# Kernel optimization log

Hardware: AMD Instinct MI355X
Metric: run time of the kernel (lower is better)

## Reference

```python
import jax, jax.numpy as jnp
import numpy as np

N, D, E, EDGE_DIM = 50000, 128, 800000, 3
NEG_SLOPE = 0.2
LN_EPS = 1e-5


def setup_inputs() -> dict:
    key = jax.random.key(0)
    ks = jax.random.split(key, 12)
    s = 1.0 / np.sqrt(D)
    return {
        "x": jax.random.normal(ks[0], (N, D), jnp.float32),
        "edge_index": jax.random.randint(ks[1], (2, E), 0, N, jnp.int32),
        "edge_attr": jax.random.normal(ks[2], (E, EDGE_DIM), jnp.float32),
        "W_l": jax.random.normal(ks[3], (D, D), jnp.float32) * s,
        "b_l": jnp.zeros((D,), jnp.float32),
        "W_r": jax.random.normal(ks[4], (D, D), jnp.float32) * s,
        "b_r": jnp.zeros((D,), jnp.float32),
        "W_e": jax.random.normal(ks[5], (EDGE_DIM, D), jnp.float32) * (1.0 / np.sqrt(EDGE_DIM)),
        "att": jax.random.normal(ks[6], (D,), jnp.float32) * s,
        "bias": jnp.zeros((D,), jnp.float32),
        "res_weight": jnp.array(0.1, jnp.float32),
        "ln_gamma": jnp.ones((D,), jnp.float32),
        "ln_beta": jnp.zeros((D,), jnp.float32),
    }


def reference(x, edge_index, edge_attr, W_l, b_l, W_r, b_r, W_e, att, bias,
              res_weight, ln_gamma, ln_beta):
    src, dst = edge_index[0], edge_index[1]
    # GATv2: lin_l on source, lin_r on target (heads=1, concat=False)
    x_l = x @ W_l + b_l            # [N, D]
    x_r = x @ W_r + b_r            # [N, D]
    e_emb = edge_attr @ W_e        # [E, D]
    # per-edge attention logits
    m = x_l[src] + x_r[dst] + e_emb                      # [E, D]
    m = jnp.where(m > 0, m, NEG_SLOPE * m)               # leaky_relu(0.2)
    alpha = m @ att                                       # [E]
    # segment softmax over destination nodes
    seg_max = jax.ops.segment_max(alpha, dst, num_segments=N)
    seg_max = jnp.where(jnp.isfinite(seg_max), seg_max, 0.0)
    ex = jnp.exp(alpha - seg_max[dst])
    seg_sum = jax.ops.segment_sum(ex, dst, num_segments=N)
    alpha = ex / (seg_sum[dst] + 1e-16)                   # [E]
    # weighted aggregation of transformed source features (dropout off / eval)
    msgs = x_l[src] * alpha[:, None]                      # [E, D]
    out = jax.ops.segment_sum(msgs, dst, num_segments=N) + bias  # [N, D]
    # residual + LayerNorm
    out = x + res_weight * out
    mu = jnp.mean(out, axis=-1, keepdims=True)
    var = jnp.mean(jnp.square(out - mu), axis=-1, keepdims=True)
    out = (out - mu) * jax.lax.rsqrt(var + LN_EPS)
    return out * ln_gamma + ln_beta
```

## Files before the change

### kernel.cpp

```cpp
#include <hip/hip_runtime.h>
#include <hip/hip_bf16.h>

#define N_NODES 50000
#define DIM 128
#define N_EDGES 800000
#define NEG_SLOPE 0.2f
#define LN_EPS 1e-5f
#define SCAN_BS 256
#define NB_SCAN ((N_NODES + SCAN_BS - 1) / SCAN_BS)


__global__ __launch_bounds__(256) void lin_kernel(
    const float* __restrict__ x,
    const float* __restrict__ Wl, const float* __restrict__ bl,
    const float* __restrict__ Wr, const float* __restrict__ br,
    __hip_bfloat16* __restrict__ xl_bf, float* __restrict__ xr)
{
    __shared__ float xs[8][DIM];
    const int node0 = blockIdx.x * 8;
    const int t = threadIdx.x;
    for (int i = t; i < 8 * DIM; i += 256) {
        int n = node0 + (i >> 7);
        xs[i >> 7][i & 127] = (n < N_NODES) ? x[(size_t)n * DIM + (i & 127)] : 0.f;
    }
    __syncthreads();
    const int d = t & 127;
    const bool is_l = (t < 128);
    const float* W = is_l ? Wl : Wr;
    const float* b = is_l ? bl : br;
    float acc[8];
#pragma unroll
    for (int i = 0; i < 8; i++) acc[i] = b[d];
    for (int k = 0; k < DIM; k++) {
        float w = W[k * DIM + d];
#pragma unroll
        for (int i = 0; i < 8; i++) acc[i] += xs[i][k] * w;
    }
#pragma unroll
    for (int i = 0; i < 8; i++) {
        int n = node0 + i;
        if (n < N_NODES) {
            if (is_l) xl_bf[(size_t)n * DIM + d] = __float2bfloat16(acc[i]);
            else      xr[(size_t)n * DIM + d] = acc[i];
        }
    }
}

__global__ __launch_bounds__(256) void hist_kernel(const int* __restrict__ dst_idx,
                                                   int* __restrict__ cnt) {
    int e = blockIdx.x * 256 + threadIdx.x;
    if (e < N_EDGES) atomicAdd(&cnt[dst_idx[e]], 1);
}

__global__ __launch_bounds__(SCAN_BS) void scan1_kernel(int* __restrict__ cnt,
                                                        int* __restrict__ partials) {
    __shared__ int sh[SCAN_BS];
    const int i = blockIdx.x * SCAN_BS + threadIdx.x;
    const int v = (i < N_NODES) ? cnt[i] : 0;
    sh[threadIdx.x] = v;
    __syncthreads();
    for (int off = 1; off < SCAN_BS; off <<= 1) {
        int t = (threadIdx.x >= off) ? sh[threadIdx.x - off] : 0;
        __syncthreads();
        sh[threadIdx.x] += t;
        __syncthreads();
    }
    if (i < N_NODES) cnt[i] = sh[threadIdx.x] - v;
    if (threadIdx.x == SCAN_BS - 1) partials[blockIdx.x] = sh[threadIdx.x];
}

__global__ __launch_bounds__(SCAN_BS) void scan2_kernel(int* __restrict__ partials) {
    __shared__ int sh[SCAN_BS];
    const int t = threadIdx.x;
    const int v = (t < NB_SCAN) ? partials[t] : 0;
    sh[t] = v;
    __syncthreads();
    for (int off = 1; off < SCAN_BS; off <<= 1) {
        int u = (t >= off) ? sh[t - off] : 0;
        __syncthreads();
        sh[t] += u;
        __syncthreads();
    }
    if (t < NB_SCAN) partials[t] = sh[t] - v;
}

__global__ __launch_bounds__(SCAN_BS) void scan3_kernel(int* __restrict__ cnt,
                                                        const int* __restrict__ partials) {
    const int i = blockIdx.x * SCAN_BS + threadIdx.x;
    if (i < N_NODES) cnt[i] += partials[blockIdx.x];
}

__global__ __launch_bounds__(256) void scatter_kernel(
    const int* __restrict__ src_idx, const int* __restrict__ dst_idx,
    const float* __restrict__ ea,
    int* __restrict__ cursor,
    int* __restrict__ sorted_src, float* __restrict__ sorted_ea) {
    int e = blockIdx.x * 256 + threadIdx.x;
    if (e >= N_EDGES) return;
    int pos = atomicAdd(&cursor[dst_idx[e]], 1);
    sorted_src[pos] = src_idx[e];
    sorted_ea[3 * pos + 0] = ea[(size_t)e * 3 + 0];
    sorted_ea[3 * pos + 1] = ea[(size_t)e * 3 + 1];
    sorted_ea[3 * pos + 2] = ea[(size_t)e * 3 + 2];
}

__global__ __launch_bounds__(256) void fused_node_kernel(
    const float* __restrict__ x, const __hip_bfloat16* __restrict__ xl_bf,
    const int* __restrict__ cursor,
    const int* __restrict__ sorted_src, const float* __restrict__ sorted_ea,
    const float* __restrict__ We, const float* __restrict__ att,
    const float* __restrict__ bias, const float* __restrict__ rw_p,
    const float* __restrict__ gamma, const float* __restrict__ beta,
    float* __restrict__ out)
{
    const int v = blockIdx.x * 4 + (threadIdx.x >> 6);
    const int lane = threadIdx.x & 63;
    if (v >= N_NODES) return;
    const int begin = (v == 0) ? 0 : cursor[v - 1];
    const int end = cursor[v];
    const size_t nb = (size_t)v * DIM + 2 * lane;
    const float2 xrv = *(const float2*)&out[nb];
    const float2 at  = *(const float2*)&att[2 * lane];
    const float2 we0 = *(const float2*)&We[0 * DIM + 2 * lane];
    const float2 we1 = *(const float2*)&We[1 * DIM + 2 * lane];
    const float2 we2 = *(const float2*)&We[2 * DIM + 2 * lane];

    float m = -3.4e38f, s = 0.f, a0 = 0.f, a1 = 0.f;
    for (int pos = begin; pos < end; ++pos) {
        const int sn = sorted_src[pos];
        const float ea0 = sorted_ea[3 * pos + 0];
        const float ea1 = sorted_ea[3 * pos + 1];
        const float ea2 = sorted_ea[3 * pos + 2];
        const unsigned xu = *(const unsigned*)&xl_bf[(size_t)sn * DIM + 2 * lane];
        const float xl0 = __uint_as_float(xu << 16);
        const float xl1 = __uint_as_float(xu & 0xffff0000u);
        float t0 = xl0 + xrv.x + ea0 * we0.x + ea1 * we1.x + ea2 * we2.x;
        float t1 = xl1 + xrv.y + ea0 * we0.y + ea1 * we1.y + ea2 * we2.y;
        t0 = t0 > 0.f ? t0 : NEG_SLOPE * t0;
        t1 = t1 > 0.f ? t1 : NEG_SLOPE * t1;
        float p = t0 * at.x + t1 * at.y;
#pragma unroll
        for (int o = 32; o > 0; o >>= 1) p += __shfl_xor(p, o, 64);
        const float mn = fmaxf(m, p);
        const float f = expf(m - mn);
        const float w = expf(p - mn);
        s  = s  * f + w;
        a0 = a0 * f + w * xl0;
        a1 = a1 * f + w * xl1;
        m = mn;
    }
    const float inv = 1.f / (s + 1e-16f);

    const float2 xv = *(const float2*)&x[nb];
    const float rw = rw_p[0];
    float v0 = xv.x + rw * (a0 * inv + bias[2 * lane]);
    float v1 = xv.y + rw * (a1 * inv + bias[2 * lane + 1]);
    float sum = v0 + v1;
#pragma unroll
    for (int o = 32; o > 0; o >>= 1) sum += __shfl_xor(sum, o, 64);
    const float mu = sum * (1.f / DIM);
    const float d0 = v0 - mu, d1 = v1 - mu;
    float q = d0 * d0 + d1 * d1;
#pragma unroll
    for (int o = 32; o > 0; o >>= 1) q += __shfl_xor(q, o, 64);
    const float rstd = rsqrtf(q * (1.f / DIM) + LN_EPS);
    float2 r;
    r.x = d0 * rstd * gamma[2 * lane]     + beta[2 * lane];
    r.y = d1 * rstd * gamma[2 * lane + 1] + beta[2 * lane + 1];
    *(float2*)&out[nb] = r;
}

extern "C" void kernel_launch(void* const* d_in, const int* in_sizes, int n_in,
                              void* d_out, int out_size, void* d_ws, size_t ws_size,
                              hipStream_t stream)
{
    const float* x    = (const float*)d_in[0];
    const int*   ei   = (const int*)d_in[1];
    const float* ea   = (const float*)d_in[2];
    const float* Wl   = (const float*)d_in[3];
    const float* bl   = (const float*)d_in[4];
    const float* Wr   = (const float*)d_in[5];
    const float* br   = (const float*)d_in[6];
    const float* We   = (const float*)d_in[7];
    const float* att  = (const float*)d_in[8];
    const float* bias = (const float*)d_in[9];
    const float* rw   = (const float*)d_in[10];
    const float* gmm  = (const float*)d_in[11];
    const float* bta  = (const float*)d_in[12];
    float* out = (float*)d_out;

    const int* src_idx = ei;
    const int* dst_idx = ei + N_EDGES;

    __hip_bfloat16* xl_bf = (__hip_bfloat16*)d_ws;
    int*   sorted_src = (int*)(xl_bf + (size_t)N_NODES * DIM);
    float* sorted_ea  = (float*)(sorted_src + N_EDGES);
    int*   cursor     = (int*)(sorted_ea + (size_t)3 * N_EDGES);
    int*   partials   = cursor + N_NODES + 64;

    hipMemsetAsync(cursor, 0, (size_t)(N_NODES + 64) * sizeof(int), stream);
    hist_kernel<<<(N_EDGES + 255) / 256, 256, 0, stream>>>(dst_idx, cursor);
    scan1_kernel<<<NB_SCAN, SCAN_BS, 0, stream>>>(cursor, partials);
    scan2_kernel<<<1, SCAN_BS, 0, stream>>>(partials);
    scan3_kernel<<<NB_SCAN, SCAN_BS, 0, stream>>>(cursor, partials);
    scatter_kernel<<<(N_EDGES + 255) / 256, 256, 0, stream>>>(src_idx, dst_idx, ea,
                                                              cursor, sorted_src, sorted_ea);
    lin_kernel<<<(N_NODES + 7) / 8, 256, 0, stream>>>(x, Wl, bl, Wr, br, xl_bf, out);
    fused_node_kernel<<<(N_NODES + 3) / 4, 256, 0, stream>>>(x, xl_bf, cursor,
                                                             sorted_src, sorted_ea,
                                                             We, att, bias, rw, gmm, bta, out);
}
```

Measured before the change: 389.9 us.

## Pad CSR rows to multiples of four and batch four edges per iteration

Each node's edge segment is padded to a multiple of four, so the node kernel can read sources and edge attributes with vector loads and process four edges per step. The four per-edge dot-product reductions share one combined shuffle tree instead of four full butterflies. The online softmax skips the rescale when the new logits are within a threshold of the running max, and uses fast __expf. This adds a padded workspace layout and a separate row-start array, and the threshold trick risks exp overflow or precision loss for large logit gaps.

```diff
diff --git a/kernel.cpp b/kernel.cpp
--- a/kernel.cpp
+++ b/kernel.cpp
@@ -8,6 +8,7 @@
 #define LN_EPS 1e-5f
 #define SCAN_BS 256
 #define NB_SCAN ((N_NODES + SCAN_BS - 1) / SCAN_BS)
+#define PADCAP (N_EDGES + 4 * N_NODES)
 
 
 __global__ __launch_bounds__(256) void lin_kernel(
@@ -56,13 +57,14 @@
                                                         int* __restrict__ partials) {
     __shared__ int sh[SCAN_BS];
     const int i = blockIdx.x * SCAN_BS + threadIdx.x;
-    const int v = (i < N_NODES) ? cnt[i] : 0;
+    const int deg = (i < N_NODES) ? cnt[i] : 0;
+    const int v = (deg + 3) & ~3;
     sh[threadIdx.x] = v;
     __syncthreads();
     for (int off = 1; off < SCAN_BS; off <<= 1) {
-        int t = (threadIdx.x >= off) ? sh[threadIdx.x - off] : 0;
-        __syncthreads();
-        sh[threadIdx.x] += t;
+        int u = (threadIdx.x >= off) ? sh[threadIdx.x - off] : 0;
+        __syncthreads();
+        sh[threadIdx.x] += u;
         __syncthreads();
     }
     if (i < N_NODES) cnt[i] = sh[threadIdx.x] - v;
@@ -85,9 +87,14 @@
 }
 
 __global__ __launch_bounds__(SCAN_BS) void scan3_kernel(int* __restrict__ cnt,
-                                                        const int* __restrict__ partials) {
+                                                        const int* __restrict__ partials,
+                                                        int* __restrict__ cursor) {
     const int i = blockIdx.x * SCAN_BS + threadIdx.x;
-    if (i < N_NODES) cnt[i] += partials[blockIdx.x];
+    if (i < N_NODES) {
+        int rs = cnt[i] + partials[blockIdx.x];
+        cnt[i] = rs;
+        cursor[i] = rs;
+    }
 }
 
 __global__ __launch_bounds__(256) void scatter_kernel(
@@ -106,7 +113,7 @@
 
 __global__ __launch_bounds__(256) void fused_node_kernel(
     const float* __restrict__ x, const __hip_bfloat16* __restrict__ xl_bf,
-    const int* __restrict__ cursor,
+    const int* __restrict__ row_start, const int* __restrict__ cursor,
     const int* __restrict__ sorted_src, const float* __restrict__ sorted_ea,
     const float* __restrict__ We, const float* __restrict__ att,
     const float* __restrict__ bias, const float* __restrict__ rw_p,
@@ -116,8 +123,8 @@
     const int v = blockIdx.x * 4 + (threadIdx.x >> 6);
     const int lane = threadIdx.x & 63;
     if (v >= N_NODES) return;
-    const int begin = (v == 0) ? 0 : cursor[v - 1];
-    const int end = cursor[v];
+    const int begin = row_start[v];
+    const int end   = cursor[v];
     const size_t nb = (size_t)v * DIM + 2 * lane;
     const float2 xrv = *(const float2*)&out[nb];
     const float2 at  = *(const float2*)&att[2 * lane];
@@ -126,7 +133,81 @@
     const float2 we2 = *(const float2*)&We[2 * DIM + 2 * lane];
 
     float m = -3.4e38f, s = 0.f, a0 = 0.f, a1 = 0.f;
-    for (int pos = begin; pos < end; ++pos) {
+    int pos = begin;
+
+    for (; pos + 4 <= end; pos += 4) {
+        const int4 s4 = *(const int4*)(sorted_src + pos);
+        const float4* eap = (const float4*)(sorted_ea + 3 * pos);
+        const float4 eA = eap[0], eB = eap[1], eC = eap[2];
+        const unsigned xu0 = *(const unsigned*)&xl_bf[(size_t)s4.x * DIM + 2 * lane];
+        const unsigned xu1 = *(const unsigned*)&xl_bf[(size_t)s4.y * DIM + 2 * lane];
+        const unsigned xu2 = *(const unsigned*)&xl_bf[(size_t)s4.z * DIM + 2 * lane];
+        const unsigned xu3 = *(const unsigned*)&xl_bf[(size_t)s4.w * DIM + 2 * lane];
+        const float xl00 = __uint_as_float(xu0 << 16), xl10 = __uint_as_float(xu0 & 0xffff0000u);
+        const float xl01 = __uint_as_float(xu1 << 16), xl11 = __uint_as_float(xu1 & 0xffff0000u);
+        const float xl02 = __uint_as_float(xu2 << 16), xl12 = __uint_as_float(xu2 & 0xffff0000u);
+        const float xl03 = __uint_as_float(xu3 << 16), xl13 = __uint_as_float(xu3 & 0xffff0000u);
+
+        float P0, P1, P2, P3;
+        {
+            float t0, t1;
+            t0 = xl00 + xrv.x + eA.x * we0.x + eA.y * we1.x + eA.z * we2.x;
+            t1 = xl10 + xrv.y + eA.x * we0.y + eA.y * we1.y + eA.z * we2.y;
+            t0 = t0 > 0.f ? t0 : NEG_SLOPE * t0;  t1 = t1 > 0.f ? t1 : NEG_SLOPE * t1;
+            P0 = t0 * at.x + t1 * at.y;
+            t0 = xl01 + xrv.x + eA.w * we0.x + eB.x * we1.x + eB.y * we2.x;
+            t1 = xl11 + xrv.y + eA.w * we0.y + eB.x * we1.y + eB.y * we2.y;
+            t0 = t0 > 0.f ? t0 : NEG_SLOPE * t0;  t1 = t1 > 0.f ? t1 : NEG_SLOPE * t1;
+            P1 = t0 * at.x + t1 * at.y;
+            t0 = xl02 + xrv.x + eB.z * we0.x + eB.w * we1.x + eC.x * we2.x;
+            t1 = xl12 + xrv.y + eB.z * we0.y + eB.w * we1.y + eC.x * we2.y;
+            t0 = t0 > 0.f ? t0 : NEG_SLOPE * t0;  t1 = t1 > 0.f ? t1 : NEG_SLOPE * t1;
+            P2 = t0 * at.x + t1 * at.y;
+            t0 = xl03 + xrv.x + eC.y * we0.x + eC.z * we1.x + eC.w * we2.x;
+            t1 = xl13 + xrv.y + eC.y * we0.y + eC.z * we1.y + eC.w * we2.y;
+            t0 = t0 > 0.f ? t0 : NEG_SLOPE * t0;  t1 = t1 > 0.f ? t1 : NEG_SLOPE * t1;
+            P3 = t0 * at.x + t1 * at.y;
+        }
+        const float tA0 = __shfl_xor(P0, 1, 64);
+        const float tA1 = __shfl_xor(P1, 1, 64);
+        const float tB0 = __shfl_xor(P2, 1, 64);
+        const float tB1 = __shfl_xor(P3, 1, 64);
+        const bool b0 = (lane & 1);
+        float A = b0 ? (P1 + tA1) : (P0 + tA0);
+        float B = b0 ? (P3 + tB1) : (P2 + tB0);
+        const float tA = __shfl_xor(A, 2, 64);
+        const float tB = __shfl_xor(B, 2, 64);
+        float C = (lane & 2) ? (B + tB) : (A + tA);
+        C += __shfl_xor(C, 4, 64);
+        C += __shfl_xor(C, 8, 64);
+        C += __shfl_xor(C, 16, 64);
+        C += __shfl_xor(C, 32, 64);
+        const int base = lane & ~3;
+        const float p0 = __shfl(C, base + 0, 64);
+        const float p1 = __shfl(C, base + 1, 64);
+        const float p2 = __shfl(C, base + 2, 64);
+        const float p3 = __shfl(C, base + 3, 64);
+
+        const float pm = fmaxf(fmaxf(p0, p1), fmaxf(p2, p3));
+        if (pm <= m + 8.f) {
+            const float w0 = __expf(p0 - m), w1 = __expf(p1 - m);
+            const float w2 = __expf(p2 - m), w3 = __expf(p3 - m);
+            s  += (w0 + w1) + (w2 + w3);
+            a0 += w0 * xl00 + w1 * xl01 + w2 * xl02 + w3 * xl03;
+            a1 += w0 * xl10 + w1 * xl11 + w2 * xl12 + w3 * xl13;
+        } else {
+            const float mn = fmaxf(m, pm);
+            const float f  = __expf(m - mn);
+            const float w0 = __expf(p0 - mn), w1 = __expf(p1 - mn);
+            const float w2 = __expf(p2 - mn), w3 = __expf(p3 - mn);
+            s  = s  * f + (w0 + w1) + (w2 + w3);
+            a0 = a0 * f + w0 * xl00 + w1 * xl01 + w2 * xl02 + w3 * xl03;
+            a1 = a1 * f + w0 * xl10 + w1 * xl11 + w2 * xl12 + w3 * xl13;
+            m = mn;
+        }
+    }
+
+    for (; pos < end; ++pos) {
         const int sn = sorted_src[pos];
         const float ea0 = sorted_ea[3 * pos + 0];
         const float ea1 = sorted_ea[3 * pos + 1];
@@ -141,14 +222,18 @@
         float p = t0 * at.x + t1 * at.y;
 #pragma unroll
         for (int o = 32; o > 0; o >>= 1) p += __shfl_xor(p, o, 64);
-        const float mn = fmaxf(m, p);
-        const float f = expf(m - mn);
-        const float w = expf(p - mn);
-        s  = s  * f + w;
-        a0 = a0 * f + w * xl0;
-        a1 = a1 * f + w * xl1;
-        m = mn;
-    }
+        if (p <= m + 8.f) {
+            const float w = __expf(p - m);
+            s += w; a0 += w * xl0; a1 += w * xl1;
+        } else {
+            const float mn = fmaxf(m, p);
+            const float f = __expf(m - mn);
+            const float w = __expf(p - mn);
+            s = s * f + w; a0 = a0 * f + w * xl0; a1 = a1 * f + w * xl1;
+            m = mn;
+        }
+    }
+
     const float inv = 1.f / (s + 1e-16f);
 
     const float2 xv = *(const float2*)&x[nb];
@@ -194,19 +279,20 @@
 
     __hip_bfloat16* xl_bf = (__hip_bfloat16*)d_ws;
     int*   sorted_src = (int*)(xl_bf + (size_t)N_NODES * DIM);
-    float* sorted_ea  = (float*)(sorted_src + N_EDGES);
-    int*   cursor     = (int*)(sorted_ea + (size_t)3 * N_EDGES);
-    int*   partials   = cursor + N_NODES + 64;
-
-    hipMemsetAsync(cursor, 0, (size_t)(N_NODES + 64) * sizeof(int), stream);
-    hist_kernel<<<(N_EDGES + 255) / 256, 256, 0, stream>>>(dst_idx, cursor);
-    scan1_kernel<<<NB_SCAN, SCAN_BS, 0, stream>>>(cursor, partials);
+    float* sorted_ea  = (float*)(sorted_src + PADCAP);
+    int*   row_start  = (int*)(sorted_ea + (size_t)3 * PADCAP);
+    int*   cursor     = row_start + N_NODES;
+    int*   partials   = cursor + N_NODES;
+
+    hipMemsetAsync(row_start, 0, (size_t)N_NODES * sizeof(int), stream);
+    hist_kernel<<<(N_EDGES + 255) / 256, 256, 0, stream>>>(dst_idx, row_start);
+    scan1_kernel<<<NB_SCAN, SCAN_BS, 0, stream>>>(row_start, partials);
     scan2_kernel<<<1, SCAN_BS, 0, stream>>>(partials);
-    scan3_kernel<<<NB_SCAN, SCAN_BS, 0, stream>>>(cursor, partials);
+    scan3_kernel<<<NB_SCAN, SCAN_BS, 0, stream>>>(row_start, partials, cursor);
     scatter_kernel<<<(N_EDGES + 255) / 256, 256, 0, stream>>>(src_idx, dst_idx, ea,
                                                               cursor, sorted_src, sorted_ea);
     lin_kernel<<<(N_NODES + 7) / 8, 256, 0, stream>>>(x, Wl, bl, Wr, br, xl_bf, out);
-    fused_node_kernel<<<(N_NODES + 3) / 4, 256, 0, stream>>>(x, xl_bf, cursor,
+    fused_node_kernel<<<(N_NODES + 3) / 4, 256, 0, stream>>>(x, xl_bf, row_start, cursor,
                                                              sorted_src, sorted_ea,
                                                              We, att, bias, rw, gmm, bta, out);
 }
```

Result: faster. 348.7 us (-10.6%).
